# Kernel tuning notes

Hardware: AMD Instinct MI355X
Metric: run time of the kernel (lower is better)

Reference implementation:

```python
import jax, jax.numpy as jnp
import numpy as np

BIG = 1e30  # finite 'inf' so masked-min keeps clean gradients

def setup_inputs() -> dict:
    key = jax.random.key(0)
    k1, k2, k3, k4 = jax.random.split(key, 4)
    B, N, C = 8, 2048, 3
    pred = jax.random.normal(k1, (B, N, C), dtype=jnp.float32)
    target = jax.random.normal(k2, (B, N, C), dtype=jnp.float32)
    points = jax.random.normal(k3, (B, N, C), dtype=jnp.float32)
    mask = jax.random.randint(k4, (B, N), 0, 2, dtype=jnp.int32)
    return {"pred": pred, "target": target, "mask": mask, "points": points}

def _loss(pred, target, points, maskf):
    # masked L1 term: per-point mean over xyz, masked mean over valid points
    l1_map = jnp.mean(jnp.abs(pred - target), axis=2) * maskf      # [B,N]
    l1 = l1_map.sum() / maskf.sum()

    clean = points + target                                        # [B,N,3]
    predp = points + pred                                          # [B,N,3]
    # pairwise L1 distances between clean (rows) and pred (cols)
    D = jnp.sum(jnp.abs(clean[:, :, None, :] - predp[:, None, :, :]), axis=-1)  # [B,N,N]

    valid_cnt = maskf.sum(axis=1)                                  # [B]
    # clean -> nearest valid pred point (mask columns j)
    min_x = jnp.min(jnp.where(maskf[:, None, :] > 0, D, BIG), axis=2)  # [B,N]
    # pred -> nearest valid clean point (mask rows i)
    min_y = jnp.min(jnp.where(maskf[:, :, None] > 0, D, BIG), axis=1)  # [B,N]
    cham = (min_x * maskf).sum(axis=1) / valid_cnt \
         + (min_y * maskf).sum(axis=1) / valid_cnt                 # [B]
    cd = cham.mean()  # per-batch chamfer summed then divided by B

    # converging_to == 'chamfer'
    return l1 + jnp.exp(-l1) * cd

def reference(pred, target, mask, points):
    maskf = mask.astype(pred.dtype)
    return _loss(pred, target, points, maskf)
```

## Files before the change

kernel.cpp:

```cpp
#include <hip/hip_runtime.h>
#include <math.h>
#include <float.h>

#define BB 8
#define NN 2048
#define BN (BB * NN)
#define BLK 256
#define Q 8
#define CSPLIT 64
#define CCHUNK (NN / CSPLIT)

#define MINPART_FLOATS (CSPLIT * 2 * BN)

__global__ __launch_bounds__(BLK) void k_main(const float* __restrict__ pred,
                                              const float* __restrict__ target,
                                              const float* __restrict__ points,
                                              const int* __restrict__ mask,
                                              float* __restrict__ minpart,
                                              float* __restrict__ l1part,
                                              float* __restrict__ cntpart,
                                              unsigned int* __restrict__ counter) {
    int bid = blockIdx.x;
    int cs = bid & (CSPLIT - 1);
    int b = (bid >> 6) & 7;
    int task = bid >> 9;
    int t = threadIdx.x;

    if (bid == 0 && t == 0) *counter = 0u;

    const float* dq = task ? pred : target;
    const float* dc = task ? target : pred;

    __shared__ float4 cand[CCHUNK];
    if (t < CCHUNK) {
        int g = b * NN + cs * CCHUNK + t;
        size_t g3 = (size_t)g * 3;
        float x = 1e30f, y = 1e30f, z = 1e30f;
        if (mask[g]) {
            x = points[g3 + 0] + dc[g3 + 0];
            y = points[g3 + 1] + dc[g3 + 1];
            z = points[g3 + 2] + dc[g3 + 2];
        }
        cand[t] = make_float4(x, y, z, 0.f);
    }
    __syncthreads();

    float qx[Q], qy[Q], qz[Q], mn[Q];
    #pragma unroll
    for (int q = 0; q < Q; ++q) {
        size_t g3 = (size_t)(b * NN + q * BLK + t) * 3;
        qx[q] = points[g3 + 0] + dq[g3 + 0];
        qy[q] = points[g3 + 1] + dq[g3 + 1];
        qz[q] = points[g3 + 2] + dq[g3 + 2];
        mn[q] = FLT_MAX;
    }

    #pragma unroll 4
    for (int j = 0; j < CCHUNK; j += 2) {
        float4 c0 = cand[j];
        float4 c1 = cand[j + 1];
        #pragma unroll
        for (int q = 0; q < Q; ++q) {
            float d0 = fabsf(qx[q] - c0.x) + fabsf(qy[q] - c0.y) + fabsf(qz[q] - c0.z);
            float d1 = fabsf(qx[q] - c1.x) + fabsf(qy[q] - c1.y) + fabsf(qz[q] - c1.z);
            mn[q] = fminf(fminf(d0, d1), mn[q]);
        }
    }

    float* mp = minpart + (size_t)cs * (2 * BN) + (size_t)task * BN + b * NN;
    #pragma unroll
    for (int q = 0; q < Q; ++q)
        mp[q * BLK + t] = mn[q];

    if (task == 0 && cs < 8) {
        int gi = b * NN + cs * BLK + t;
        size_t g3 = (size_t)gi * 3;
        float m = (float)mask[gi];
        float s = (fabsf(pred[g3 + 0] - target[g3 + 0]) +
                   fabsf(pred[g3 + 1] - target[g3 + 1]) +
                   fabsf(pred[g3 + 2] - target[g3 + 2])) * (1.0f / 3.0f) * m;
        float c = m;
        for (int off = 32; off; off >>= 1) {
            s += __shfl_down(s, off, 64);
            c += __shfl_down(c, off, 64);
        }
        __shared__ float ls[4], lc[4];
        if ((t & 63) == 0) { ls[t >> 6] = s; lc[t >> 6] = c; }
        __syncthreads();
        if (t == 0) {
            l1part[b * 8 + cs]  = ls[0] + ls[1] + ls[2] + ls[3];
            cntpart[b * 8 + cs] = lc[0] + lc[1] + lc[2] + lc[3];
        }
    }
}

__global__ __launch_bounds__(BLK) void k_redfin(const float* __restrict__ minpart,
                                                const int* __restrict__ mask,
                                                const float* __restrict__ l1part,
                                                const float* __restrict__ cntpart,
                                                float* __restrict__ champart,
                                                unsigned int* __restrict__ counter,
                                                float* __restrict__ out) {
    int tb = blockIdx.x;
    int s4 = tb & 3;
    int b = (tb >> 2) & 7;
    int task = tb >> 5;
    int t = threadIdx.x;

    float v = 0.f;
    #pragma unroll
    for (int k = 0; k < 2; ++k) {
        int qi = s4 * 512 + k * BLK + t;
        size_t idx = (size_t)task * BN + b * NN + qi;
        float mn = minpart[idx];
        #pragma unroll
        for (int cs = 1; cs < CSPLIT; ++cs)
            mn = fminf(mn, minpart[(size_t)cs * (2 * BN) + idx]);
        v += mn * (float)mask[b * NN + qi];
    }
    for (int off = 32; off; off >>= 1) v += __shfl_down(v, off, 64);

    __shared__ float ls[4];
    __shared__ int isLast;
    __shared__ float ch[64];
    if ((t & 63) == 0) ls[t >> 6] = v;
    __syncthreads();
    if (t == 0) {
        float bs = ls[0] + ls[1] + ls[2] + ls[3];
        __hip_atomic_store(&champart[tb], bs, __ATOMIC_RELEASE, __HIP_MEMORY_SCOPE_AGENT);
        int ticket = __hip_atomic_fetch_add(counter, 1u, __ATOMIC_ACQ_REL, __HIP_MEMORY_SCOPE_AGENT);
        isLast = (ticket == 63);
    }
    __syncthreads();
    if (!isLast) return;

    if (t < 64) ch[t] = __hip_atomic_load(&champart[t], __ATOMIC_ACQUIRE, __HIP_MEMORY_SCOPE_AGENT);
    __syncthreads();
    if (t == 0) {
        double cnt[BB], msum = 0.0, l1num = 0.0;
        for (int b2 = 0; b2 < BB; ++b2) {
            double cb = 0.0;
            for (int k = 0; k < 8; ++k) {
                cb += (double)cntpart[b2 * 8 + k];
                l1num += (double)l1part[b2 * 8 + k];
            }
            cnt[b2] = cb;
            msum += cb;
        }
        double l1 = l1num / msum;
        double cd = 0.0;
        for (int b2 = 0; b2 < BB; ++b2) {
            double chb = 0.0;
            for (int tk = 0; tk < 2; ++tk)
                for (int s = 0; s < 4; ++s)
                    chb += (double)ch[tk * 32 + b2 * 4 + s];
            cd += chb / cnt[b2];
        }
        cd *= (1.0 / BB);
        out[0] = (float)(l1 + exp(-l1) * cd);
    }
}

extern "C" void kernel_launch(void* const* d_in, const int* in_sizes, int n_in,
                              void* d_out, int out_size, void* d_ws, size_t ws_size,
                              hipStream_t stream) {
    const float* pred   = (const float*)d_in[0];
    const float* target = (const float*)d_in[1];
    const int*   mask   = (const int*)d_in[2];
    const float* points = (const float*)d_in[3];
    float* out = (float*)d_out;

    float* minpart  = (float*)d_ws;
    char* tail = (char*)d_ws + (size_t)MINPART_FLOATS * 4;
    float* champart = (float*)tail;
    float* l1part   = (float*)(tail + 256);
    float* cntpart  = (float*)(tail + 512);
    unsigned int* counter = (unsigned int*)(tail + 768);

    k_main<<<2 * BB * CSPLIT, BLK, 0, stream>>>(pred, target, points, mask,
                                                minpart, l1part, cntpart, counter);
    k_redfin<<<64, BLK, 0, stream>>>(minpart, mask, l1part, cntpart,
                                     champart, counter, out);
}
```

Baseline: 26.52 us.

## Split query points across blocks and shrink candidate split to cut partial-min traffic

Changes the work decomposition of the main kernel. Each block now handles 2 query points per thread over a quarter of the points, with 16 candidate chunks of 128 instead of 64 chunks of 32. The grid size stays the same, but the partial-min buffer written and re-read by the reduction kernel shrinks fourfold, and the reduction kernel does 15 fminf loads per element across 128 blocks instead of 63 across 64. The trade-off is less register reuse of each candidate load across query points and more redundant candidate staging across query slices.

```diff
diff --git a/kernel.cpp b/kernel.cpp
--- a/kernel.cpp
+++ b/kernel.cpp
@@ -6,8 +6,10 @@
 #define NN 2048
 #define BN (BB * NN)
 #define BLK 256
-#define Q 8
-#define CSPLIT 64
+#define Q 2
+#define QSPLIT 4
+#define QSLICE (BLK * Q)
+#define CSPLIT 16
 #define CCHUNK (NN / CSPLIT)
 
 #define MINPART_FLOATS (CSPLIT * 2 * BN)
@@ -22,6 +24,7 @@
                                               unsigned int* __restrict__ counter) {
     int bid = blockIdx.x;
     int cs = bid & (CSPLIT - 1);
+    int qs = (bid >> 4) & (QSPLIT - 1);
     int b = (bid >> 6) & 7;
     int task = bid >> 9;
     int t = threadIdx.x;
@@ -48,14 +51,15 @@
     float qx[Q], qy[Q], qz[Q], mn[Q];
     #pragma unroll
     for (int q = 0; q < Q; ++q) {
-        size_t g3 = (size_t)(b * NN + q * BLK + t) * 3;
+        int qi = qs * QSLICE + q * BLK + t;
+        size_t g3 = (size_t)(b * NN + qi) * 3;
         qx[q] = points[g3 + 0] + dq[g3 + 0];
         qy[q] = points[g3 + 1] + dq[g3 + 1];
         qz[q] = points[g3 + 2] + dq[g3 + 2];
         mn[q] = FLT_MAX;
     }
 
-    #pragma unroll 4
+    #pragma unroll 8
     for (int j = 0; j < CCHUNK; j += 2) {
         float4 c0 = cand[j];
         float4 c1 = cand[j + 1];
@@ -70,16 +74,20 @@
     float* mp = minpart + (size_t)cs * (2 * BN) + (size_t)task * BN + b * NN;
     #pragma unroll
     for (int q = 0; q < Q; ++q)
-        mp[q * BLK + t] = mn[q];
+        mp[qs * QSLICE + q * BLK + t] = mn[q];
 
-    if (task == 0 && cs < 8) {
-        int gi = b * NN + cs * BLK + t;
-        size_t g3 = (size_t)gi * 3;
-        float m = (float)mask[gi];
-        float s = (fabsf(pred[g3 + 0] - target[g3 + 0]) +
-                   fabsf(pred[g3 + 1] - target[g3 + 1]) +
-                   fabsf(pred[g3 + 2] - target[g3 + 2])) * (1.0f / 3.0f) * m;
-        float c = m;
+    if (task == 0 && cs == 0) {
+        float s = 0.f, c = 0.f;
+        #pragma unroll
+        for (int q = 0; q < Q; ++q) {
+            int gi = b * NN + qs * QSLICE + q * BLK + t;
+            size_t g3 = (size_t)gi * 3;
+            float m = (float)mask[gi];
+            s += (fabsf(pred[g3 + 0] - target[g3 + 0]) +
+                  fabsf(pred[g3 + 1] - target[g3 + 1]) +
+                  fabsf(pred[g3 + 2] - target[g3 + 2])) * (1.0f / 3.0f) * m;
+            c += m;
+        }
         for (int off = 32; off; off >>= 1) {
             s += __shfl_down(s, off, 64);
             c += __shfl_down(c, off, 64);
@@ -88,8 +96,8 @@
         if ((t & 63) == 0) { ls[t >> 6] = s; lc[t >> 6] = c; }
         __syncthreads();
         if (t == 0) {
-            l1part[b * 8 + cs]  = ls[0] + ls[1] + ls[2] + ls[3];
-            cntpart[b * 8 + cs] = lc[0] + lc[1] + lc[2] + lc[3];
+            l1part[b * QSPLIT + qs]  = ls[0] + ls[1] + ls[2] + ls[3];
+            cntpart[b * QSPLIT + qs] = lc[0] + lc[1] + lc[2] + lc[3];
         }
     }
 }
@@ -102,47 +110,44 @@
                                                 unsigned int* __restrict__ counter,
                                                 float* __restrict__ out) {
     int tb = blockIdx.x;
-    int s4 = tb & 3;
-    int b = (tb >> 2) & 7;
-    int task = tb >> 5;
+    int s8 = tb & 7;
+    int b = (tb >> 3) & 7;
+    int task = tb >> 6;
     int t = threadIdx.x;
 
-    float v = 0.f;
+    int qi = s8 * BLK + t;
+    size_t idx = (size_t)task * BN + b * NN + qi;
+    float mn = minpart[idx];
     #pragma unroll
-    for (int k = 0; k < 2; ++k) {
-        int qi = s4 * 512 + k * BLK + t;
-        size_t idx = (size_t)task * BN + b * NN + qi;
-        float mn = minpart[idx];
-        #pragma unroll
-        for (int cs = 1; cs < CSPLIT; ++cs)
-            mn = fminf(mn, minpart[(size_t)cs * (2 * BN) + idx]);
-        v += mn * (float)mask[b * NN + qi];
-    }
+    for (int cs = 1; cs < CSPLIT; ++cs)
+        mn = fminf(mn, minpart[(size_t)cs * (2 * BN) + idx]);
+    float v = mn * (float)mask[b * NN + qi];
+
     for (int off = 32; off; off >>= 1) v += __shfl_down(v, off, 64);
 
     __shared__ float ls[4];
     __shared__ int isLast;
-    __shared__ float ch[64];
+    __shared__ float ch[128];
     if ((t & 63) == 0) ls[t >> 6] = v;
     __syncthreads();
     if (t == 0) {
         float bs = ls[0] + ls[1] + ls[2] + ls[3];
         __hip_atomic_store(&champart[tb], bs, __ATOMIC_RELEASE, __HIP_MEMORY_SCOPE_AGENT);
         int ticket = __hip_atomic_fetch_add(counter, 1u, __ATOMIC_ACQ_REL, __HIP_MEMORY_SCOPE_AGENT);
-        isLast = (ticket == 63);
+        isLast = (ticket == 127);
     }
     __syncthreads();
     if (!isLast) return;
 
-    if (t < 64) ch[t] = __hip_atomic_load(&champart[t], __ATOMIC_ACQUIRE, __HIP_MEMORY_SCOPE_AGENT);
+    if (t < 128) ch[t] = __hip_atomic_load(&champart[t], __ATOMIC_ACQUIRE, __HIP_MEMORY_SCOPE_AGENT);
     __syncthreads();
     if (t == 0) {
         double cnt[BB], msum = 0.0, l1num = 0.0;
         for (int b2 = 0; b2 < BB; ++b2) {
             double cb = 0.0;
-            for (int k = 0; k < 8; ++k) {
-                cb += (double)cntpart[b2 * 8 + k];
-                l1num += (double)l1part[b2 * 8 + k];
+            for (int k = 0; k < QSPLIT; ++k) {
+                cb += (double)cntpart[b2 * QSPLIT + k];
+                l1num += (double)l1part[b2 * QSPLIT + k];
             }
             cnt[b2] = cb;
             msum += cb;
@@ -152,8 +157,8 @@
         for (int b2 = 0; b2 < BB; ++b2) {
             double chb = 0.0;
             for (int tk = 0; tk < 2; ++tk)
-                for (int s = 0; s < 4; ++s)
-                    chb += (double)ch[tk * 32 + b2 * 4 + s];
+                for (int s = 0; s < 8; ++s)
+                    chb += (double)ch[tk * 64 + b2 * 8 + s];
             cd += chb / cnt[b2];
         }
         cd *= (1.0 / BB);
@@ -173,12 +178,12 @@
     float* minpart  = (float*)d_ws;
     char* tail = (char*)d_ws + (size_t)MINPART_FLOATS * 4;
     float* champart = (float*)tail;
-    float* l1part   = (float*)(tail + 256);
-    float* cntpart  = (float*)(tail + 512);
+    float* l1part   = (float*)(tail + 512);
+    float* cntpart  = (float*)(tail + 640);
     unsigned int* counter = (unsigned int*)(tail + 768);
 
-    k_main<<<2 * BB * CSPLIT, BLK, 0, stream>>>(pred, target, points, mask,
-                                                minpart, l1part, cntpart, counter);
-    k_redfin<<<64, BLK, 0, stream>>>(minpart, mask, l1part, cntpart,
-                                     champart, counter, out);
+    k_main<<<2 * BB * QSPLIT * CSPLIT, BLK, 0, stream>>>(pred, target, points, mask,
+                                                         minpart, l1part, cntpart, counter);
+    k_redfin<<<128, BLK, 0, stream>>>(minpart, mask, l1part, cntpart,
+                                      champart, counter, out);
 }
```

Result: faster. 23.64 us (-10.9%).
